# Optimization experiments

Measured on AMD Instinct MI355X. Metric: run time of the kernel, lower is better.

The kernel has to match this reference:

```python
import jax, jax.numpy as jnp
import numpy as np

NUM_IMU = 72
NUM_NOISE = 12
MAX_PROP = 300
LN_EPS = 1e-5

def _softplus(x):
    return jax.nn.softplus(x)

def setup_inputs() -> dict:
    key = jax.random.key(0)
    k1, k2, k3, k4, k5 = jax.random.split(key, 5)
    d_model = 1024
    seq_len = 4096
    hidden_states = jax.random.normal(k1, (1, seq_len, d_model), dtype=jnp.float32)
    ln_gamma = jnp.ones((d_model,), dtype=jnp.float32)
    ln_beta = jnp.zeros((d_model,), dtype=jnp.float32)
    # Linear: d_model -> NUM_IMU * NUM_NOISE
    W = jax.random.normal(k2, (d_model, NUM_IMU * NUM_NOISE), dtype=jnp.float32) / np.sqrt(d_model)
    b = jax.random.normal(k3, (NUM_IMU * NUM_NOISE,), dtype=jnp.float32) * 0.01
    return {"hidden_states": hidden_states, "ln_gamma": ln_gamma, "ln_beta": ln_beta, "W": W, "b": b}

def _forward(hidden_states, ln_gamma, ln_beta, W, b):
    seq_len = hidden_states.shape[1]
    tsteps = min(MAX_PROP, seq_len)
    x = hidden_states[0]  # [seq, d_model] (squeeze batch=1)
    mu = jnp.mean(x, axis=-1, keepdims=True)
    var = jnp.mean((x - mu) ** 2, axis=-1, keepdims=True)
    xn = (x - mu) * jax.lax.rsqrt(var + LN_EPS) * ln_gamma + ln_beta
    # noise params: [seq, NUM_NOISE, NUM_IMU]
    p = (xn @ W + b).reshape(seq_len, NUM_NOISE, NUM_IMU)
    c = p[:, 4, :]
    c_theta = p[:, 5, :]
    phi = p[:, 6, :]
    phi_theta = p[:, 7, :]
    d = _softplus(p[:, 1, :])
    k = d ** 2 / 4 + _softplus(p[:, 0, :])
    d_theta = _softplus(p[:, 3, :])
    k_theta = d_theta ** 2 / 4 + _softplus(p[:, 2, :])
    acc_base = p[:, 8, :].T      # [imu, seq]
    acc_std = _softplus(p[:, 9, :]).T
    gyro_base = p[:, 10, :].T
    gyro_std = _softplus(p[:, 11, :]).T
    # vectorize over imu: move to [imu, seq, 1]
    def I(a):
        return a.T[:, :, None]
    t = jnp.arange(tsteps, dtype=jnp.float32)[None, None, :]  # [1,1,tstep]
    k_, d_, phi_, c_ = I(k), I(d), I(phi), I(c)
    kt_, dt_, pht_, ct_ = I(k_theta), I(d_theta), I(phi_theta), I(c_theta)
    omega1 = jnp.sqrt(k_ * 4 - d_ ** 2) / 2
    lin = c_ * jnp.exp(-d_ / 2 * t) * jnp.sin(t * omega1 + phi_)
    omega2 = jnp.sqrt(kt_ * 4 - dt_ ** 2) / 2
    ang = ct_ * jnp.exp(-dt_ / 2 * t) * jnp.sin(t * omega2 + pht_)
    spring = lin + ang  # [imu, seq, tstep]
    # banded scatter-add: out[s+t] += spring[:, s, t] for s+t < seq_len
    pos = jnp.arange(seq_len, dtype=jnp.int32)[:, None] + jnp.arange(tsteps, dtype=jnp.int32)[None, :]
    pos_flat = pos.reshape(-1)
    mask = pos_flat < seq_len
    pos_safe = jnp.where(mask, pos_flat, 0)
    vals = spring.reshape(NUM_IMU, -1) * mask.astype(spring.dtype)
    kinematics = jnp.zeros((NUM_IMU, seq_len), dtype=spring.dtype).at[:, pos_safe].add(vals)
    return kinematics, acc_base, acc_std, gyro_base, gyro_std

def reference(hidden_states, ln_gamma, ln_beta, W, b):
    return _forward(hidden_states, ln_gamma, ln_beta, W, b)
```

## Files before the change

### kernel.cpp

```cpp
#include <hip/hip_runtime.h>
#include <hip/hip_bf16.h>
#include <math.h>

#define SEQ 4096
#define DM  1024
#define NIMU 72
#define NNOISE 12
#define NJ (NIMU*NNOISE)
#define TSTEPS 300
#define PLANE (NIMU*SEQ)

#define A2F_SHORTS ((size_t)256 * 64 * 512)
#define BTF_SHORTS ((size_t)56 * 64 * 512)

typedef __attribute__((ext_vector_type(8))) short bf16x8;
typedef __attribute__((ext_vector_type(4))) float f32x4;
typedef __attribute__((ext_vector_type(2))) float f32x2;

__device__ __forceinline__ float softplus_f(float x) {
    return fmaxf(x, 0.f) + log1pf(expf(-fabsf(x)));
}

__device__ __forceinline__ void split_bf16(float x, short& hi, short& lo) {
    unsigned b = __float_as_uint(x);
    unsigned h = (b + 0x7FFFu + ((b >> 16) & 1u)) >> 16;
    float hf = __uint_as_float(h << 16);
    float r = x - hf;
    unsigned b2 = __float_as_uint(r);
    unsigned l2 = (b2 + 0x7FFFu + ((b2 >> 16) & 1u)) >> 16;
    hi = (short)h;
    lo = (short)l2;
}

__global__ __launch_bounds__(1024) void ln_kernel(const float* __restrict__ x,
                                                  const float* __restrict__ gamma,
                                                  const float* __restrict__ beta,
                                                  short* __restrict__ A2f) {
    const int s_tile = blockIdx.x;
    const int tid = threadIdx.x;
    const int mrow = tid >> 6;
    const int g    = tid & 63;
    const int row  = s_tile * 16 + mrow;
    const float4* xr = (const float4*)(x + (size_t)row * DM);

    float s = 0.f, sq = 0.f;
    #pragma unroll
    for (int i = 0; i < 4; ++i) {
        float4 v = xr[g + 64 * i];
        s  += v.x + v.y + v.z + v.w;
        sq += v.x*v.x + v.y*v.y + v.z*v.z + v.w*v.w;
    }
    #pragma unroll
    for (int off = 1; off < 64; off <<= 1) {
        s  += __shfl_xor(s, off);
        sq += __shfl_xor(sq, off);
    }
    const float mean = s * (1.f / DM);
    const float var  = sq * (1.f / DM) - mean * mean;
    const float rstd = rsqrtf(fmaxf(var, 0.f) + 1e-5f);

    #pragma unroll
    for (int i = 0; i < 4; ++i) {
        const int c4 = g + 64 * i;
        float4 v = xr[c4];
        float4 gm = ((const float4*)gamma)[c4];
        float4 bt = ((const float4*)beta)[c4];
        float o[4];
        o[0] = (v.x - mean) * rstd * gm.x + bt.x;
        o[1] = (v.y - mean) * rstd * gm.y + bt.y;
        o[2] = (v.z - mean) * rstd * gm.z + bt.z;
        o[3] = (v.w - mean) * rstd * gm.w + bt.w;
        short4 hv, lv;
        split_bf16(o[0], hv.x, lv.x);
        split_bf16(o[1], hv.y, lv.y);
        split_bf16(o[2], hv.z, lv.z);
        split_bf16(o[3], hv.w, lv.w);
        const int ch = c4 >> 3;
        const size_t base = ((size_t)s_tile * 64 + ch) * 512
                          + mrow * 8 + ((c4 >> 1) & 3) * 128 + (c4 & 1) * 4;
        *(short4*)(A2f + base)             = hv;
        *(short4*)(A2f + base + 32 * 512)  = lv;
    }
}

__global__ __launch_bounds__(256) void wprep_kernel(const float* __restrict__ W,
                                                    short* __restrict__ Btf) {
    __shared__ float T[32][33];
    const int k0 = blockIdx.x * 32, j0 = blockIdx.y * 32;
    const int t = threadIdx.x;
    {
        const int r = t >> 3, c4 = (t & 7) * 4;
        float4 v = *(const float4*)(W + (size_t)(k0 + r) * NJ + j0 + c4);
        T[r][c4 + 0] = v.x; T[r][c4 + 1] = v.y; T[r][c4 + 2] = v.z; T[r][c4 + 3] = v.w;
    }
    __syncthreads();
    if (t < 128) {
        const int gq = t >> 6;
        const int l  = t & 63;
        const int n = l & 15, c = l >> 4;
        const int jt = blockIdx.y * 2 + gq;
        bf16x8 hv, lv;
        #pragma unroll
        for (int o = 0; o < 8; ++o) {
            short h, lo_;
            split_bf16(T[c * 8 + o][gq * 16 + n], h, lo_);
            hv[o] = h; lv[o] = lo_;
        }
        short* dh = Btf + ((size_t)jt * 64 + blockIdx.x) * 512 + l * 8;
        *(bf16x8*)dh = hv;
        *(bf16x8*)(dh + (size_t)32 * 512) = lv;
    }
}

__global__ __launch_bounds__(512, 4) void gemm_kernel(const short* __restrict__ A2f,
                                                      const short* __restrict__ Btf,
                                                      const float* __restrict__ bias,
                                                      float* __restrict__ pt,
                                                      float* __restrict__ out) {
    const int bid = blockIdx.x;
    const int c = bid & 7, u = bid >> 3;
    const int bxi = u / 7;
    const int by = u - bxi * 7;
    const int bx = c * 8 + bxi;
    const int l = threadIdx.x & 63, w = threadIdx.x >> 6;
    const int wm = w & 1, wj = w >> 1;
    const int st0 = bx * 4 + wm * 2;
    const int jt0 = by * 8 + wj * 2;
    const short* aB = A2f + (size_t)st0 * (64 * 512) + l * 8;
    const short* bB = Btf + (size_t)jt0 * (64 * 512) + l * 8;

    f32x4 acc[2][2] = {};
    bf16x8 ah[2][2], al[2][2], bh[2][2], bl[2][2];

    auto ldstep = [&](int slot, int i) {
        #pragma unroll
        for (int t = 0; t < 2; ++t) {
            ah[slot][t] = *(const bf16x8*)(aB + ((size_t)t * 64 + i) * 512);
            al[slot][t] = *(const bf16x8*)(aB + ((size_t)t * 64 + 32 + i) * 512);
            bh[slot][t] = *(const bf16x8*)(bB + ((size_t)t * 64 + i) * 512);
            bl[slot][t] = *(const bf16x8*)(bB + ((size_t)t * 64 + 32 + i) * 512);
        }
    };

    ldstep(0, 0);
    #pragma unroll 2
    for (int i = 0; i < 32; ++i) {
        const int cur = i & 1;
        if (i + 1 < 32) ldstep(cur ^ 1, i + 1);
        #pragma unroll
        for (int mi = 0; mi < 2; ++mi)
            #pragma unroll
            for (int ni = 0; ni < 2; ++ni)
                acc[mi][ni] = __builtin_amdgcn_mfma_f32_16x16x32_bf16(
                    ah[cur][mi], bh[cur][ni], acc[mi][ni], 0, 0, 0);
        #pragma unroll
        for (int mi = 0; mi < 2; ++mi)
            #pragma unroll
            for (int ni = 0; ni < 2; ++ni)
                acc[mi][ni] = __builtin_amdgcn_mfma_f32_16x16x32_bf16(
                    ah[cur][mi], bl[cur][ni], acc[mi][ni], 0, 0, 0);
        #pragma unroll
        for (int mi = 0; mi < 2; ++mi)
            #pragma unroll
            for (int ni = 0; ni < 2; ++ni)
                acc[mi][ni] = __builtin_amdgcn_mfma_f32_16x16x32_bf16(
                    al[cur][mi], bh[cur][ni], acc[mi][ni], 0, 0, 0);
    }

    const int srow = (l >> 4) * 4;
    const int jcol = l & 15;
    #pragma unroll
    for (int ni = 0; ni < 2; ++ni) {
        const int jt = jt0 + ni;
        const int j = jt * 16 + jcol;
        if (j < NJ) {
            const float bj = bias[j];
            if (jt < 36) {
                #pragma unroll
                for (int mi = 0; mi < 2; ++mi) {
                    f32x4 v = acc[mi][ni];
                    v[0] += bj; v[1] += bj; v[2] += bj; v[3] += bj;
                    *(f32x4*)(pt + (size_t)j * SEQ + (st0 + mi) * 16 + srow) = v;
                }
            } else {
                const int noise = j / 72;
                const int imu = j - noise * 72;
                float* dst = out + (size_t)(noise - 7) * PLANE + (size_t)imu * SEQ;
                const bool sp = (noise & 1);
                #pragma unroll
                for (int mi = 0; mi < 2; ++mi) {
                    f32x4 v = acc[mi][ni];
                    v[0] += bj; v[1] += bj; v[2] += bj; v[3] += bj;
                    if (sp) {
                        v[0] = softplus_f(v[0]); v[1] = softplus_f(v[1]);
                        v[2] = softplus_f(v[2]); v[3] = softplus_f(v[3]);
                    }
                    *(f32x4*)(dst + (st0 + mi) * 16 + srow) = v;
                }
            }
        }
    }
}

__global__ __launch_bounds__(256) void spring_kernel(const float* __restrict__ pt,
                                                     float* __restrict__ kin) {
    __shared__ float w3[3][4 * 368];
    const int tid  = threadIdx.x;
    const int lane = tid & 63;
    const int wid  = tid >> 6;
    const int s0   = blockIdx.x * 256;
    const int imu  = blockIdx.y;
    const int s    = s0 + (wid << 6) + lane;

    #pragma unroll
    for (int b = 0; b < 3; ++b)
        #pragma unroll
        for (int i = 0; i < 6; ++i) {
            const int idx = lane + i * 64;
            if (idx < 363) w3[b][wid * 368 + idx] = 0.f;
        }

    const int base = imu * SEQ + s;
    const float p0  = pt[(size_t)0 * PLANE + base];
    const float p1  = pt[(size_t)1 * PLANE + base];
    const float p2  = pt[(size_t)2 * PLANE + base];
    const float p3  = pt[(size_t)3 * PLANE + base];
    const float c1  = pt[(size_t)4 * PLANE + base];
    const float c2  = pt[(size_t)5 * PLANE + base];
    const float ph1 = pt[(size_t)6 * PLANE + base];
    const float ph2 = pt[(size_t)7 * PLANE + base];

    float dd = softplus_f(p1);
    float kk = dd * dd * 0.25f + softplus_f(p0);
    float om1 = 0.5f * sqrtf(fmaxf(4.f * kk - dd * dd, 0.f));
    float dt = softplus_f(p3);
    float kt = dt * dt * 0.25f + softplus_f(p2);
    float om2 = 0.5f * sqrtf(fmaxf(4.f * kt - dt * dt, 0.f));
    float e1 = expf(-0.5f * dd), e2 = expf(-0.5f * dt);
    float sn, cs, sn2, cs2;
    sincosf(om1, &sn, &cs);
    sincosf(om2, &sn2, &cs2);
    f32x2 Rr = {e1 * cs, e2 * cs2};
    f32x2 Ri = {e1 * sn, e2 * sn2};
    sincosf(ph1, &sn, &cs);
    sincosf(ph2, &sn2, &cs2);
    f32x2 zr = {c1 * cs, c2 * cs2};
    f32x2 zi = {c1 * sn, c2 * sn2};

    f32x2 zrB, ziB;
    {
        f32x2 prr = Rr, pri = Ri;
        f32x2 qr = {1.f, 1.f}, qi = {0.f, 0.f};
        int e = 150;
        while (e) {
            if (e & 1) {
                f32x2 nr = qr * prr - qi * pri;
                qi = qr * pri + qi * prr;
                qr = nr;
            }
            f32x2 nr = prr * prr - pri * pri;
            pri = 2.f * prr * pri;
            prr = nr;
            e >>= 1;
        }
        f32x2 nr = zr * qr - zi * qi;
        ziB = zr * qi + zi * qr;
        zrB = nr;
    }

    float* q0 = &w3[0][wid * 368 + lane];
    float* q1 = &w3[1][wid * 368 + lane];
    float* q2 = &w3[2][wid * 368 + lane];

    #pragma unroll 1
    for (int j = 0; j < 150; j += 3) {
        float vA0 = zi.x + zi.y;
        { f32x2 nr = zr * Rr - zi * Ri; zi = zr * Ri + zi * Rr; zr = nr; }
        float vA1 = zi.x + zi.y;
        { f32x2 nr = zr * Rr - zi * Ri; zi = zr * Ri + zi * Rr; zr = nr; }
        float vA2 = zi.x + zi.y;
        { f32x2 nr = zr * Rr - zi * Ri; zi = zr * Ri + zi * Rr; zr = nr; }
        float vB0 = ziB.x + ziB.y;
        { f32x2 nr = zrB * Rr - ziB * Ri; ziB = zrB * Ri + ziB * Rr; zrB = nr; }
        float vB1 = ziB.x + ziB.y;
        { f32x2 nr = zrB * Rr - ziB * Ri; ziB = zrB * Ri + ziB * Rr; zrB = nr; }
        float vB2 = ziB.x + ziB.y;
        { f32x2 nr = zrB * Rr - ziB * Ri; ziB = zrB * Ri + ziB * Rr; zrB = nr; }

        const float a0 = q0[j],     b0 = q0[j + 150];
        const float a1 = q1[j + 1], b1 = q1[j + 151];
        const float a2 = q2[j + 2], b2 = q2[j + 152];
        q0[j]       = a0 + vA0;  q0[j + 150] = b0 + vB0;
        q1[j + 1]   = a1 + vA1;  q1[j + 151] = b1 + vB1;
        q2[j + 2]   = a2 + vA2;  q2[j + 152] = b2 + vB2;
        __asm__ volatile("" ::: "memory");
    }

    __syncthreads();
    for (int i = tid; i < 555; i += 256) {
        float sum = 0.f;
        #pragma unroll
        for (int w = 0; w < 4; ++w) {
            const int idx = i - (w << 6);
            if (idx >= 0 && idx < 363) {
                const int o = w * 368 + idx;
                sum += w3[0][o] + w3[1][o] + w3[2][o];
            }
        }
        const int pos = s0 + i;
        if (pos < SEQ) {
            (void)__hip_atomic_fetch_add(&kin[(size_t)imu * SEQ + pos], sum,
                                         __ATOMIC_RELAXED, __HIP_MEMORY_SCOPE_AGENT);
        }
    }
}

extern "C" void kernel_launch(void* const* d_in, const int* in_sizes, int n_in,
                              void* d_out, int out_size, void* d_ws, size_t ws_size,
                              hipStream_t stream) {
    const float* hs    = (const float*)d_in[0];
    const float* gamma = (const float*)d_in[1];
    const float* beta  = (const float*)d_in[2];
    const float* W     = (const float*)d_in[3];
    const float* b     = (const float*)d_in[4];
    float* out = (float*)d_out;

    short* A2f = (short*)d_ws;
    short* Btf = A2f + A2F_SHORTS;
    float* pt  = (float*)(Btf + BTF_SHORTS);

    hipMemsetAsync(out, 0, (size_t)PLANE * sizeof(float), stream);

    ln_kernel<<<SEQ / 16, 1024, 0, stream>>>(hs, gamma, beta, A2f);
    wprep_kernel<<<dim3(DM / 32, NJ / 32), 256, 0, stream>>>(W, Btf);
    gemm_kernel<<<448, 512, 0, stream>>>(A2f, Btf, b, pt, out);
    spring_kernel<<<dim3(SEQ / 256, NIMU), 256, 0, stream>>>(pt, out);
}
```

Before: 150.6 us.

## Switch GEMM to 32x32 MFMA with split-K and separate tail epilogue

Reorganizes the A and B bf16 fragment layouts for 32x32x16 MFMA and splits the K dimension across two block groups that write separate partial buffers. The spring kernel sums the two partials, and a new tail kernel sums and softplus-transforms the base/std planes. The layernorm kernel is re-tiled to 32 threads per row. This aims at better MFMA efficiency and occupancy, at the cost of doubled partial-result traffic, an extra launch and a larger workspace.

Result: faster. 144.0 us (-4.4%).

```diff
diff --git a/kernel.cpp b/kernel.cpp
--- a/kernel.cpp
+++ b/kernel.cpp
@@ -10,10 +10,11 @@
 #define TSTEPS 300
 #define PLANE (NIMU*SEQ)
 
-#define A2F_SHORTS ((size_t)256 * 64 * 512)
-#define BTF_SHORTS ((size_t)56 * 64 * 512)
+#define A2F_SHORTS ((size_t)128 * 128 * 512)
+#define BTF_SHORTS ((size_t)28 * 128 * 512)
 
 typedef __attribute__((ext_vector_type(8))) short bf16x8;
+typedef __attribute__((ext_vector_type(16))) float f32x16;
 typedef __attribute__((ext_vector_type(4))) float f32x4;
 typedef __attribute__((ext_vector_type(2))) float f32x2;
 
@@ -32,26 +33,24 @@
     lo = (short)l2;
 }
 
-__global__ __launch_bounds__(1024) void ln_kernel(const float* __restrict__ x,
-                                                  const float* __restrict__ gamma,
-                                                  const float* __restrict__ beta,
-                                                  short* __restrict__ A2f) {
-    const int s_tile = blockIdx.x;
+__global__ __launch_bounds__(512) void ln_kernel(const float* __restrict__ x,
+                                                 const float* __restrict__ gamma,
+                                                 const float* __restrict__ beta,
+                                                 short* __restrict__ A2f) {
     const int tid = threadIdx.x;
-    const int mrow = tid >> 6;
-    const int g    = tid & 63;
-    const int row  = s_tile * 16 + mrow;
+    const int row = blockIdx.x * 16 + (tid >> 5);
+    const int c   = tid & 31;
     const float4* xr = (const float4*)(x + (size_t)row * DM);
 
     float s = 0.f, sq = 0.f;
     #pragma unroll
-    for (int i = 0; i < 4; ++i) {
-        float4 v = xr[g + 64 * i];
+    for (int i = 0; i < 8; ++i) {
+        float4 v = xr[c + 32 * i];
         s  += v.x + v.y + v.z + v.w;
         sq += v.x*v.x + v.y*v.y + v.z*v.z + v.w*v.w;
     }
     #pragma unroll
-    for (int off = 1; off < 64; off <<= 1) {
+    for (int off = 1; off < 32; off <<= 1) {
         s  += __shfl_xor(s, off);
         sq += __shfl_xor(sq, off);
     }
@@ -59,10 +58,11 @@
     const float var  = sq * (1.f / DM) - mean * mean;
     const float rstd = rsqrtf(fmaxf(var, 0.f) + 1e-5f);
 
-    #pragma unroll
-    for (int i = 0; i < 4; ++i) {
-        const int c4 = g + 64 * i;
-        float4 v = xr[c4];
+    const int s_tile = row >> 5, r = row & 31;
+    #pragma unroll
+    for (int i = 0; i < 8; ++i) {
+        const int c4 = c + 32 * i;
+        float4 v  = xr[c4];
         float4 gm = ((const float4*)gamma)[c4];
         float4 bt = ((const float4*)beta)[c4];
         float o[4];
@@ -75,11 +75,12 @@
         split_bf16(o[1], hv.y, lv.y);
         split_bf16(o[2], hv.z, lv.z);
         split_bf16(o[3], hv.w, lv.w);
-        const int ch = c4 >> 3;
-        const size_t base = ((size_t)s_tile * 64 + ch) * 512
-                          + mrow * 8 + ((c4 >> 1) & 3) * 128 + (c4 & 1) * 4;
-        *(short4*)(A2f + base)             = hv;
-        *(short4*)(A2f + base + 32 * 512)  = lv;
+        const int ch = c4 >> 2;
+        const int g  = (c4 >> 1) & 1;
+        const int o4 = (c4 & 1) * 4;
+        const size_t base = ((size_t)s_tile * 128 + ch) * 512 + (g * 32 + r) * 8 + o4;
+        *(short4*)(A2f + base)                    = hv;
+        *(short4*)(A2f + base + (size_t)64 * 512) = lv;
     }
 }
 
@@ -95,50 +96,52 @@
     }
     __syncthreads();
     if (t < 128) {
-        const int gq = t >> 6;
-        const int l  = t & 63;
-        const int n = l & 15, c = l >> 4;
-        const int jt = blockIdx.y * 2 + gq;
+        const int q = t >> 6;
+        const int l = t & 63;
+        const int n = l & 31, g = l >> 5;
+        const int jt = blockIdx.y;
+        const int ch = blockIdx.x * 2 + q;
         bf16x8 hv, lv;
         #pragma unroll
         for (int o = 0; o < 8; ++o) {
             short h, lo_;
-            split_bf16(T[c * 8 + o][gq * 16 + n], h, lo_);
+            split_bf16(T[q * 16 + g * 8 + o][n], h, lo_);
             hv[o] = h; lv[o] = lo_;
         }
-        short* dh = Btf + ((size_t)jt * 64 + blockIdx.x) * 512 + l * 8;
+        short* dh = Btf + ((size_t)jt * 128 + ch) * 512 + l * 8;
         *(bf16x8*)dh = hv;
-        *(bf16x8*)(dh + (size_t)32 * 512) = lv;
-    }
-}
-
-__global__ __launch_bounds__(512, 4) void gemm_kernel(const short* __restrict__ A2f,
+        *(bf16x8*)(dh + (size_t)64 * 512) = lv;
+    }
+}
+
+__global__ __launch_bounds__(256, 2) void gemm_kernel(const short* __restrict__ A2f,
                                                       const short* __restrict__ Btf,
                                                       const float* __restrict__ bias,
-                                                      float* __restrict__ pt,
-                                                      float* __restrict__ out) {
+                                                      float* __restrict__ ptA,
+                                                      float* __restrict__ ptB) {
     const int bid = blockIdx.x;
     const int c = bid & 7, u = bid >> 3;
-    const int bxi = u / 7;
-    const int by = u - bxi * 7;
-    const int bx = c * 8 + bxi;
+    const int kh = u / 28, v = u - kh * 28;
+    const int bxi = v / 7, by = v - bxi * 7;
+    const int bx = c * 4 + bxi;
     const int l = threadIdx.x & 63, w = threadIdx.x >> 6;
-    const int wm = w & 1, wj = w >> 1;
-    const int st0 = bx * 4 + wm * 2;
-    const int jt0 = by * 8 + wj * 2;
-    const short* aB = A2f + (size_t)st0 * (64 * 512) + l * 8;
-    const short* bB = Btf + (size_t)jt0 * (64 * 512) + l * 8;
-
-    f32x4 acc[2][2] = {};
+    const int mt0 = bx * 4 + (w & 1) * 2;
+    const int jt0 = by * 4 + (w >> 1) * 2;
+    const int ch0 = kh * 32;
+    const short* aB = A2f + (size_t)mt0 * (128 * 512) + l * 8;
+    const short* bB = Btf + (size_t)jt0 * (128 * 512) + l * 8;
+
+    f32x16 acc[2][2] = {};
     bf16x8 ah[2][2], al[2][2], bh[2][2], bl[2][2];
 
     auto ldstep = [&](int slot, int i) {
+        const size_t chh = ch0 + i, chl = chh + 64;
         #pragma unroll
         for (int t = 0; t < 2; ++t) {
-            ah[slot][t] = *(const bf16x8*)(aB + ((size_t)t * 64 + i) * 512);
-            al[slot][t] = *(const bf16x8*)(aB + ((size_t)t * 64 + 32 + i) * 512);
-            bh[slot][t] = *(const bf16x8*)(bB + ((size_t)t * 64 + i) * 512);
-            bl[slot][t] = *(const bf16x8*)(bB + ((size_t)t * 64 + 32 + i) * 512);
+            ah[slot][t] = *(const bf16x8*)(aB + ((size_t)t * 128 + chh) * 512);
+            al[slot][t] = *(const bf16x8*)(aB + ((size_t)t * 128 + chl) * 512);
+            bh[slot][t] = *(const bf16x8*)(bB + ((size_t)t * 128 + chh) * 512);
+            bl[slot][t] = *(const bf16x8*)(bB + ((size_t)t * 128 + chl) * 512);
         }
     };
 
@@ -151,58 +154,49 @@
         for (int mi = 0; mi < 2; ++mi)
             #pragma unroll
             for (int ni = 0; ni < 2; ++ni)
-                acc[mi][ni] = __builtin_amdgcn_mfma_f32_16x16x32_bf16(
+                acc[mi][ni] = __builtin_amdgcn_mfma_f32_32x32x16_bf16(
                     ah[cur][mi], bh[cur][ni], acc[mi][ni], 0, 0, 0);
         #pragma unroll
         for (int mi = 0; mi < 2; ++mi)
             #pragma unroll
             for (int ni = 0; ni < 2; ++ni)
-                acc[mi][ni] = __builtin_amdgcn_mfma_f32_16x16x32_bf16(
+                acc[mi][ni] = __builtin_amdgcn_mfma_f32_32x32x16_bf16(
                     ah[cur][mi], bl[cur][ni], acc[mi][ni], 0, 0, 0);
         #pragma unroll
         for (int mi = 0; mi < 2; ++mi)
             #pragma unroll
             for (int ni = 0; ni < 2; ++ni)
-                acc[mi][ni] = __builtin_amdgcn_mfma_f32_16x16x32_bf16(
+                acc[mi][ni] = __builtin_amdgcn_mfma_f32_32x32x16_bf16(
                     al[cur][mi], bh[cur][ni], acc[mi][ni], 0, 0, 0);
     }
 
-    const int srow = (l >> 4) * 4;
-    const int jcol = l & 15;
+    float* ptH = kh ? ptB : ptA;
+    const int jn = l & 31, hi5 = l >> 5;
     #pragma unroll
     for (int ni = 0; ni < 2; ++ni) {
         const int jt = jt0 + ni;
-        const int j = jt * 16 + jcol;
-        if (j < NJ) {
-            const float bj = bias[j];
-            if (jt < 36) {
+        if (jt < 27) {
+            const int j = jt * 32 + jn;
+            const float bj = (kh == 0) ? bias[j] : 0.f;
+            #pragma unroll
+            for (int mi = 0; mi < 2; ++mi) {
                 #pragma unroll
-                for (int mi = 0; mi < 2; ++mi) {
-                    f32x4 v = acc[mi][ni];
-                    v[0] += bj; v[1] += bj; v[2] += bj; v[3] += bj;
-                    *(f32x4*)(pt + (size_t)j * SEQ + (st0 + mi) * 16 + srow) = v;
-                }
-            } else {
-                const int noise = j / 72;
-                const int imu = j - noise * 72;
-                float* dst = out + (size_t)(noise - 7) * PLANE + (size_t)imu * SEQ;
-                const bool sp = (noise & 1);
-                #pragma unroll
-                for (int mi = 0; mi < 2; ++mi) {
-                    f32x4 v = acc[mi][ni];
-                    v[0] += bj; v[1] += bj; v[2] += bj; v[3] += bj;
-                    if (sp) {
-                        v[0] = softplus_f(v[0]); v[1] = softplus_f(v[1]);
-                        v[2] = softplus_f(v[2]); v[3] = softplus_f(v[3]);
-                    }
-                    *(f32x4*)(dst + (st0 + mi) * 16 + srow) = v;
+                for (int q = 0; q < 4; ++q) {
+                    f32x4 o;
+                    o[0] = acc[mi][ni][q * 4 + 0] + bj;
+                    o[1] = acc[mi][ni][q * 4 + 1] + bj;
+                    o[2] = acc[mi][ni][q * 4 + 2] + bj;
+                    o[3] = acc[mi][ni][q * 4 + 3] + bj;
+                    const int s = (mt0 + mi) * 32 + q * 8 + hi5 * 4;
+                    *(f32x4*)(ptH + (size_t)j * SEQ + s) = o;
                 }
             }
         }
     }
 }
 
-__global__ __launch_bounds__(256) void spring_kernel(const float* __restrict__ pt,
+__global__ __launch_bounds__(256) void spring_kernel(const float* __restrict__ ptA,
+                                                     const float* __restrict__ ptB,
                                                      float* __restrict__ kin) {
     __shared__ float w3[3][4 * 368];
     const int tid  = threadIdx.x;
@@ -221,14 +215,14 @@
         }
 
     const int base = imu * SEQ + s;
-    const float p0  = pt[(size_t)0 * PLANE + base];
-    const float p1  = pt[(size_t)1 * PLANE + base];
-    const float p2  = pt[(size_t)2 * PLANE + base];
-    const float p3  = pt[(size_t)3 * PLANE + base];
-    const float c1  = pt[(size_t)4 * PLANE + base];
-    const float c2  = pt[(size_t)5 * PLANE + base];
-    const float ph1 = pt[(size_t)6 * PLANE + base];
-    const float ph2 = pt[(size_t)7 * PLANE + base];
+    const float p0  = ptA[(size_t)0 * PLANE + base] + ptB[(size_t)0 * PLANE + base];
+    const float p1  = ptA[(size_t)1 * PLANE + base] + ptB[(size_t)1 * PLANE + base];
+    const float p2  = ptA[(size_t)2 * PLANE + base] + ptB[(size_t)2 * PLANE + base];
+    const float p3  = ptA[(size_t)3 * PLANE + base] + ptB[(size_t)3 * PLANE + base];
+    const float c1  = ptA[(size_t)4 * PLANE + base] + ptB[(size_t)4 * PLANE + base];
+    const float c2  = ptA[(size_t)5 * PLANE + base] + ptB[(size_t)5 * PLANE + base];
+    const float ph1 = ptA[(size_t)6 * PLANE + base] + ptB[(size_t)6 * PLANE + base];
+    const float ph2 = ptA[(size_t)7 * PLANE + base] + ptB[(size_t)7 * PLANE + base];
 
     float dd = softplus_f(p1);
     float kk = dd * dd * 0.25f + softplus_f(p0);
@@ -315,6 +309,23 @@
     }
 }
 
+__global__ __launch_bounds__(256) void tail_kernel(const float* __restrict__ ptA,
+                                                   const float* __restrict__ ptB,
+                                                   float* __restrict__ out) {
+    const int i4 = blockIdx.x * 256 + threadIdx.x;
+    if (i4 >= PLANE) return;
+    const float4 a = ((const float4*)(ptA + (size_t)8 * PLANE))[i4];
+    const float4 b = ((const float4*)(ptB + (size_t)8 * PLANE))[i4];
+    float4 v;
+    v.x = a.x + b.x; v.y = a.y + b.y; v.z = a.z + b.z; v.w = a.w + b.w;
+    const int q = (int)(((size_t)i4 * 4) / PLANE);
+    if (q & 1) {
+        v.x = softplus_f(v.x); v.y = softplus_f(v.y);
+        v.z = softplus_f(v.z); v.w = softplus_f(v.w);
+    }
+    ((float4*)(out + (size_t)PLANE))[i4] = v;
+}
+
 extern "C" void kernel_launch(void* const* d_in, const int* in_sizes, int n_in,
                               void* d_out, int out_size, void* d_ws, size_t ws_size,
                               hipStream_t stream) {
@@ -327,12 +338,14 @@
 
     short* A2f = (short*)d_ws;
     short* Btf = A2f + A2F_SHORTS;
-    float* pt  = (float*)(Btf + BTF_SHORTS);
+    float* ptA = (float*)(Btf + BTF_SHORTS);
+    float* ptB = ptA + (size_t)12 * PLANE;
 
     hipMemsetAsync(out, 0, (size_t)PLANE * sizeof(float), stream);
 
-    ln_kernel<<<SEQ / 16, 1024, 0, stream>>>(hs, gamma, beta, A2f);
+    ln_kernel<<<SEQ / 16, 512, 0, stream>>>(hs, gamma, beta, A2f);
     wprep_kernel<<<dim3(DM / 32, NJ / 32), 256, 0, stream>>>(W, Btf);
-    gemm_kernel<<<448, 512, 0, stream>>>(A2f, Btf, b, pt, out);
-    spring_kernel<<<dim3(SEQ / 256, NIMU), 256, 0, stream>>>(pt, out);
-}
+    gemm_kernel<<<448, 256, 0, stream>>>(A2f, Btf, b, ptA, ptB);
+    spring_kernel<<<dim3(SEQ / 256, NIMU), 256, 0, stream>>>(ptA, ptB, out);
+    tail_kernel<<<(PLANE + 255) / 256, 256, 0, stream>>>(ptA, ptB, out);
+}
```
